# Optimization experiments

Hardware: AMD Instinct MI355X
Metric: run time of the kernel (lower is better)

Reference implementation:

```python
import jax, jax.numpy as jnp
import numpy as np

D = 512   # d_model
K = 24    # decode steps
B = 8192  # batch


def setup_inputs() -> dict:
    key = jax.random.key(0)
    ks = jax.random.split(key, 10)
    s = 1.0 / np.sqrt(D)
    return {
        "initial": jax.random.normal(ks[0], (B, 1, 1), jnp.float32),
        "encoder_hidden": jax.random.normal(ks[1], (B, D), jnp.float32) * 0.1,
        "encoder_cell": jax.random.normal(ks[2], (B, D), jnp.float32) * 0.1,
        # LSTM params: input dim is 1 (feedback of dense1 output); gate order i,f,g,o (Keras)
        "Wx": jax.random.normal(ks[3], (1, 4 * D), jnp.float32) * s,
        "Wu": jax.random.normal(ks[4], (D, 4 * D), jnp.float32) * s,
        "b": jnp.zeros((4 * D,), jnp.float32),
        "w1": jax.random.normal(ks[5], (D, 1), jnp.float32) * s,
        "b1": jnp.zeros((1,), jnp.float32),
        "w2": jax.random.normal(ks[6], (D, 1), jnp.float32) * s,
        "b2": jnp.zeros((1,), jnp.float32),
    }


def reference(initial, encoder_hidden, encoder_cell, Wx, Wu, b, w1, b1, w2, b2):
    """Autoregressive LSTM decode: step 0 consumes `initial`, then feeds dense1
    output back as the next LSTM input; state carries across all K steps."""

    def step(carry, _):
        x, h, c = carry                      # x:[B,1], h,c:[B,D]
        z = x @ Wx + h @ Wu + b              # [B,4D]
        i, f, g, o = jnp.split(z, 4, axis=-1)
        i = jax.nn.sigmoid(i)
        f = jax.nn.sigmoid(f)
        g = jnp.tanh(g)
        o = jax.nn.sigmoid(o)
        c = f * c + i * g
        h = o * jnp.tanh(c)
        y1 = jax.nn.sigmoid(h @ w1 + b1)     # dense1, feedback input
        y2 = jax.nn.elu(h @ w2 + b2)         # dense2
        return (y1, h, c), (y1, y2)

    x0 = initial[:, 0, :]                    # [B,1]
    _, (ys1, ys2) = jax.lax.scan(step, (x0, encoder_hidden, encoder_cell), None, length=K)
    out1 = jnp.transpose(ys1[..., 0], (1, 0))  # [B,K]
    out2 = jnp.transpose(ys2[..., 0], (1, 0))  # [B,K]
    return out1, out2
```

## Files before the change

### kernel.cpp

```cpp
#include <hip/hip_runtime.h>

#define D_ 512
#define ND_ 2048
#define KS_ 24
#define TB_ 32
#define B_ 8192
#define NU_ 33

typedef __attribute__((ext_vector_type(8))) short short8;
typedef __attribute__((ext_vector_type(16))) float f32x16;
typedef unsigned short u16;

#define SWZ(row, kb) (((row) * 1024) + ((kb) ^ (((row) & 15) << 4)))

__device__ __forceinline__ u16 f2bf(float f) {
  union { float f; unsigned int u; } v; v.f = f;
  unsigned int u = v.u;
  return (u16)((u + 0x7FFFu + ((u >> 16) & 1u)) >> 16);
}

__device__ __forceinline__ float sigm(float x) { return 1.0f / (1.0f + __expf(-x)); }
__device__ __forceinline__ float tanh_(float x) {
  float e = __expf(2.0f * x);
  return (e - 1.0f) / (e + 1.0f);
}

__device__ __forceinline__ void glds16(const u16* g, void* l) {
  __builtin_amdgcn_global_load_lds(
      (const __attribute__((address_space(1))) unsigned int*)g,
      (__attribute__((address_space(3))) unsigned int*)l, 16, 0, 0);
}

__global__ __launch_bounds__(256) void pack_wu_kernel(const float* __restrict__ Wu,
                                                      const float* __restrict__ Wx,
                                                      const float* __restrict__ b,
                                                      u16* __restrict__ pk) {
  int idx = blockIdx.x * 256 + threadIdx.x;
  int lane = idx & 63;
  int unit = idx >> 6;
  if (unit >= 64 * NU_) return;
  int nt = unit / NU_;
  int un = unit - nt * NU_;
  int col = nt * 32 + (lane & 31);
  u16 t[8] = {0, 0, 0, 0, 0, 0, 0, 0};
  if (un < 32) {
    int k0 = un * 16 + (lane >> 5) * 8;
#pragma unroll
    for (int j = 0; j < 8; ++j) t[j] = f2bf(Wu[(size_t)(k0 + j) * ND_ + col]);
  } else if ((lane >> 5) == 0) {
    t[0] = f2bf(Wx[col]);
    t[1] = f2bf(b[col]);
  }
  int4 w;
  w.x = t[0] | (t[1] << 16); w.y = t[2] | (t[3] << 16);
  w.z = t[4] | (t[5] << 16); w.w = t[6] | (t[7] << 16);
  *reinterpret_cast<int4*>(pk + (size_t)unit * 512 + lane * 8) = w;
}

__global__ __launch_bounds__(1024, 4) void lstm_kernel(
    const float* __restrict__ initial, const float* __restrict__ enc_h,
    const float* __restrict__ enc_c,
    const float* __restrict__ w1, const float* __restrict__ b1,
    const float* __restrict__ w2, const float* __restrict__ b2,
    const u16* __restrict__ wu, float* __restrict__ out) {
  __shared__ __align__(16) unsigned char hbuf[2][TB_ * 1024];
  __shared__ __align__(16) unsigned char wu_stage[16 * 4096];
  __shared__ float x_lds[TB_];
  __shared__ float ly1[16][TB_];
  __shared__ float ly2[16][TB_];

  const int tid = threadIdx.x;
  const int wv  = tid >> 6;
  const int wvu = __builtin_amdgcn_readfirstlane(wv);
  const int l   = tid & 63;
  const int l31 = l & 31;
  const int lhi = l >> 5;
  const int b0  = blockIdx.x * TB_;

  {
    int row = tid >> 5;
    int seg = tid & 31;
    const float* src = enc_h + (size_t)(b0 + row) * D_ + seg * 16;
#pragma unroll
    for (int jb = 0; jb < 2; ++jb) {
      u16 t[8];
#pragma unroll
      for (int j = 0; j < 8; ++j) t[j] = f2bf(src[jb * 8 + j]);
      int kb = seg * 32 + jb * 16;
      int4 w;
      w.x = t[0] | (t[1] << 16); w.y = t[2] | (t[3] << 16);
      w.z = t[4] | (t[5] << 16); w.w = t[6] | (t[7] << 16);
      *reinterpret_cast<int4*>(&hbuf[0][SWZ(row, kb)]) = w;
    }
  }
  if (tid < TB_) x_lds[tid] = initial[b0 + tid];

  const int col = wvu * 32 + l31;
  const float w1v = w1[col], w2v = w2[col];
  const float b1v = b1[0], b2v = b2[0];

  float creg[16];
#pragma unroll
  for (int r = 0; r < 16; ++r) {
    const int row = (r & 3) + 8 * (r >> 2) + 4 * lhi;
    creg[r] = enc_c[(size_t)(b0 + row) * D_ + col];
  }

  const u16* wb0 = wu + (size_t)(( 0 + wvu) * NU_) * 512;
  const u16* wb1 = wu + (size_t)((16 + wvu) * NU_) * 512;
  const u16* wb2 = wu + (size_t)((32 + wvu) * NU_) * 512;
  const u16* wb3 = wu + (size_t)((48 + wvu) * NU_) * 512;
  const size_t lofs8 = (size_t)l * 8;

  unsigned char* stg = &wu_stage[wvu * 4096];
  const int lofs = l * 16;
  const int abase = lhi * 16;

  __syncthreads();

  for (int s = 0; s < KS_; ++s) {
    const unsigned char* hr = hbuf[s & 1];
    unsigned char* hw = hbuf[(s & 1) ^ 1];

    f32x16 acc0 = {}, acc1 = {}, acc2 = {}, acc3 = {};

    glds16(wb0 + lofs8, stg);
    glds16(wb1 + lofs8, stg + 1024);

#pragma unroll 1
    for (int ks = 0; ks <= 32; ++ks) {
      const size_t o = (size_t)ks * 512 + lofs8;
      glds16(wb2 + o, stg + 2048);
      glds16(wb3 + o, stg + 3072);
      asm volatile("s_waitcnt vmcnt(2)" ::: "memory");
      short8 a;
      if (ks < 32) {
        a = *reinterpret_cast<const short8*>(&hr[SWZ(l31, ks * 32 + abase)]);
      } else {
        short8 z8 = {};
        a = z8;
        if (lhi == 0) {
          a[0] = (short)f2bf(x_lds[l31]);
          a[1] = (short)0x3F80;
        }
      }
      short8 f0 = *reinterpret_cast<const short8*>(stg + lofs);
      short8 f1 = *reinterpret_cast<const short8*>(stg + 1024 + lofs);
      acc0 = __builtin_amdgcn_mfma_f32_32x32x16_bf16(a, f0, acc0, 0, 0, 0);
      acc1 = __builtin_amdgcn_mfma_f32_32x32x16_bf16(a, f1, acc1, 0, 0, 0);
      if (ks < 32) {
        const size_t o2 = (size_t)(ks + 1) * 512 + lofs8;
        glds16(wb0 + o2, stg);
        glds16(wb1 + o2, stg + 1024);
        asm volatile("s_waitcnt vmcnt(2)" ::: "memory");
      } else {
        asm volatile("s_waitcnt vmcnt(0)" ::: "memory");
      }
      short8 f2 = *reinterpret_cast<const short8*>(stg + 2048 + lofs);
      short8 f3 = *reinterpret_cast<const short8*>(stg + 3072 + lofs);
      acc2 = __builtin_amdgcn_mfma_f32_32x32x16_bf16(a, f2, acc2, 0, 0, 0);
      acc3 = __builtin_amdgcn_mfma_f32_32x32x16_bf16(a, f3, acc3, 0, 0, 0);
    }

#pragma unroll
    for (int rb = 0; rb < 16; rb += 4) {
      float y1t[4], y2t[4];
#pragma unroll
      for (int q = 0; q < 4; ++q) {
        const int r = rb + q;
        const int row = (r & 3) + 8 * (r >> 2) + 4 * lhi;
        float ig = sigm(acc0[r]);
        float fg = sigm(acc1[r]);
        float gg = tanh_(acc2[r]);
        float og = sigm(acc3[r]);
        float cn = fg * creg[r] + ig * gg;
        creg[r] = cn;
        float hn = og * tanh_(cn);
        *reinterpret_cast<u16*>(&hw[SWZ(row, col * 2)]) = f2bf(hn);
        y1t[q] = hn * w1v;
        y2t[q] = hn * w2v;
      }
#pragma unroll
      for (int m = 1; m < 32; m <<= 1) {
#pragma unroll
        for (int q = 0; q < 4; ++q) {
          y1t[q] += __shfl_xor(y1t[q], m);
          y2t[q] += __shfl_xor(y2t[q], m);
        }
      }
      if (l31 == 0) {
#pragma unroll
        for (int q = 0; q < 4; ++q) {
          const int r = rb + q;
          const int row = (r & 3) + 8 * (r >> 2) + 4 * lhi;
          ly1[wvu][row] = y1t[q];
          ly2[wvu][row] = y2t[q];
        }
      }
    }
    __syncthreads();

    if (tid < TB_) {
      float s1 = b1v, s2 = b2v;
#pragma unroll
      for (int wq = 0; wq < 16; ++wq) { s1 += ly1[wq][tid]; s2 += ly2[wq][tid]; }
      float y1 = sigm(s1);
      float y2 = (s2 > 0.f) ? s2 : (__expf(s2) - 1.0f);
      out[(size_t)(b0 + tid) * KS_ + s] = y1;
      out[(size_t)B_ * KS_ + (size_t)(b0 + tid) * KS_ + s] = y2;
      x_lds[tid] = y1;
    }
    __syncthreads();
  }
}

extern "C" void kernel_launch(void* const* d_in, const int* in_sizes, int n_in,
                              void* d_out, int out_size, void* d_ws, size_t ws_size,
                              hipStream_t stream) {
  const float* initial = (const float*)d_in[0];
  const float* enc_h   = (const float*)d_in[1];
  const float* enc_c   = (const float*)d_in[2];
  const float* Wx      = (const float*)d_in[3];
  const float* Wu      = (const float*)d_in[4];
  const float* bias    = (const float*)d_in[5];
  const float* w1      = (const float*)d_in[6];
  const float* b1      = (const float*)d_in[7];
  const float* w2      = (const float*)d_in[8];
  const float* b2      = (const float*)d_in[9];
  u16* pk = (u16*)d_ws;

  pack_wu_kernel<<<528, 256, 0, stream>>>(Wu, Wx, bias, pk);
  lstm_kernel<<<256, 1024, 0, stream>>>(initial, enc_h, enc_c, w1, b1,
                                        w2, b2, pk, (float*)d_out);
}
```

Measured before the change: 834.8 us.

## Halve waves per block, two column tiles per wave, deeper continuous weight prefetch ring

Each block now runs 8 waves instead of 16, and each wave handles two 32-column tiles in sequence, A then B. Weight staging becomes a 5-slot ring buffer per wave, and prefetch runs continuously across the passes and decode steps, so the next tile's weights are already loading at the end of each pass. The dense-head partial sums are reduced once per step over both tiles, with half as many LDS partials. This aims to hide global weight-load latency with deeper prefetch and to cut the number of waves taking part in barriers. In exchange it doubles the serial work per wave, uses more registers for two cell-state arrays and the partial-sum arrays, and relies on carefully tracked vmcnt counts.

```diff
diff --git a/kernel.cpp b/kernel.cpp
--- a/kernel.cpp
+++ b/kernel.cpp
@@ -57,17 +57,73 @@
   *reinterpret_cast<int4*>(pk + (size_t)unit * 512 + lane * 8) = w;
 }
 
-__global__ __launch_bounds__(1024, 4) void lstm_kernel(
+#define KSTEP_PASS(CREG, COL, W1V, W2V, A0, A1, A2, A3, X0, X1, X2, X3)        \
+  {                                                                            \
+    acc0 = (f32x16){}; acc1 = (f32x16){}; acc2 = (f32x16){}; acc3 = (f32x16){};\
+    _Pragma("unroll 1")                                                        \
+    for (int ks = 0; ks < 33; ++ks) {                                          \
+      int iks = ks + 2; int swp = 0;                                           \
+      if (iks >= 33) { iks -= 33; swp = 1; }                                   \
+      const size_t io = (size_t)iks * 512 + lofs8;                             \
+                        \
+      glds16((swp ? X0 : A0) + io, stg + slot_i * 2048);                       \
+      glds16((swp ? X1 : A1) + io, stg + slot_i * 2048 + 1024);                \
+      slot_i = (slot_i == 4) ? 0 : slot_i + 1;                                 \
+      asm volatile("s_waitcnt vmcnt(8)" ::: "memory");                         \
+      short8 a;                                                                \
+      if (ks < 32) {                                                           \
+        a = *reinterpret_cast<const short8*>(&hr[SWZ(l31, ks * 32 + abase)]);  \
+      } else {                                                                 \
+        short8 z8 = {};                                                        \
+        if (lhi == 0) {                                                        \
+          z8[0] = (short)f2bf(x_lds[l31]);                                     \
+          z8[1] = (short)0x3F80;                                               \
+        }                                                                      \
+        a = z8;                                                                \
+      }                                                                        \
+      short8 f0 = *reinterpret_cast<const short8*>(stg + slot_c * 2048 + lofs);\
+      short8 f1 = *reinterpret_cast<const short8*>(stg + slot_c * 2048 + 1024 + lofs);\
+      slot_c = (slot_c == 4) ? 0 : slot_c + 1;                                 \
+      acc0 = __builtin_amdgcn_mfma_f32_32x32x16_bf16(a, f0, acc0, 0, 0, 0);    \
+      acc1 = __builtin_amdgcn_mfma_f32_32x32x16_bf16(a, f1, acc1, 0, 0, 0);    \
+                                                                     \
+      glds16((swp ? X2 : A2) + io, stg + slot_i * 2048);                       \
+      glds16((swp ? X3 : A3) + io, stg + slot_i * 2048 + 1024);                \
+      slot_i = (slot_i == 4) ? 0 : slot_i + 1;                                 \
+      asm volatile("s_waitcnt vmcnt(8)" ::: "memory");                         \
+      short8 f2 = *reinterpret_cast<const short8*>(stg + slot_c * 2048 + lofs);\
+      short8 f3 = *reinterpret_cast<const short8*>(stg + slot_c * 2048 + 1024 + lofs);\
+      slot_c = (slot_c == 4) ? 0 : slot_c + 1;                                 \
+      acc2 = __builtin_amdgcn_mfma_f32_32x32x16_bf16(a, f2, acc2, 0, 0, 0);    \
+      acc3 = __builtin_amdgcn_mfma_f32_32x32x16_bf16(a, f3, acc3, 0, 0, 0);    \
+    }                                                                          \
+    _Pragma("unroll")                                                          \
+    for (int r = 0; r < 16; ++r) {                                             \
+      const int row = (r & 3) + 8 * (r >> 2) + 4 * lhi;                        \
+      float ig = sigm(acc0[r]);                                                \
+      float fg = sigm(acc1[r]);                                                \
+      float gg = tanh_(acc2[r]);                                               \
+      float og = sigm(acc3[r]);                                                \
+      float cn = fg * CREG[r] + ig * gg;                                       \
+      CREG[r] = cn;                                                            \
+      float hn = og * tanh_(cn);                                               \
+      *reinterpret_cast<u16*>(&hw[SWZ(row, (COL) * 2)]) = f2bf(hn);            \
+      y1p[r] += hn * (W1V);                                                    \
+      y2p[r] += hn * (W2V);                                                    \
+    }                                                                          \
+  }
+
+__global__ __launch_bounds__(512, 2) void lstm_kernel(
     const float* __restrict__ initial, const float* __restrict__ enc_h,
     const float* __restrict__ enc_c,
     const float* __restrict__ w1, const float* __restrict__ b1,
     const float* __restrict__ w2, const float* __restrict__ b2,
     const u16* __restrict__ wu, float* __restrict__ out) {
   __shared__ __align__(16) unsigned char hbuf[2][TB_ * 1024];
-  __shared__ __align__(16) unsigned char wu_stage[16 * 4096];
+  __shared__ __align__(16) unsigned char wu_stage[8 * 5 * 2048];
   __shared__ float x_lds[TB_];
-  __shared__ float ly1[16][TB_];
-  __shared__ float ly2[16][TB_];
+  __shared__ float ly1[8][TB_];
+  __shared__ float ly2[8][TB_];
 
   const int tid = threadIdx.x;
   const int wv  = tid >> 6;
@@ -78,15 +134,15 @@
   const int b0  = blockIdx.x * TB_;
 
   {
-    int row = tid >> 5;
-    int seg = tid & 31;
-    const float* src = enc_h + (size_t)(b0 + row) * D_ + seg * 16;
-#pragma unroll
-    for (int jb = 0; jb < 2; ++jb) {
+    int row = tid >> 4;
+    int seg = tid & 15;
+    const float* src = enc_h + (size_t)(b0 + row) * D_ + seg * 32;
+#pragma unroll
+    for (int jb = 0; jb < 4; ++jb) {
       u16 t[8];
 #pragma unroll
       for (int j = 0; j < 8; ++j) t[j] = f2bf(src[jb * 8 + j]);
-      int kb = seg * 32 + jb * 16;
+      int kb = seg * 64 + jb * 16;
       int4 w;
       w.x = t[0] | (t[1] << 16); w.y = t[2] | (t[3] << 16);
       w.z = t[4] | (t[5] << 16); w.w = t[6] | (t[7] << 16);
@@ -95,107 +151,72 @@
   }
   if (tid < TB_) x_lds[tid] = initial[b0 + tid];
 
-  const int col = wvu * 32 + l31;
-  const float w1v = w1[col], w2v = w2[col];
+  const int colA = wvu * 32 + l31;
+  const int colB = (8 + wvu) * 32 + l31;
+  const float w1vA = w1[colA], w1vB = w1[colB];
+  const float w2vA = w2[colA], w2vB = w2[colB];
   const float b1v = b1[0], b2v = b2[0];
 
-  float creg[16];
+  float cregA[16], cregB[16];
 #pragma unroll
   for (int r = 0; r < 16; ++r) {
     const int row = (r & 3) + 8 * (r >> 2) + 4 * lhi;
-    creg[r] = enc_c[(size_t)(b0 + row) * D_ + col];
-  }
-
-  const u16* wb0 = wu + (size_t)(( 0 + wvu) * NU_) * 512;
-  const u16* wb1 = wu + (size_t)((16 + wvu) * NU_) * 512;
-  const u16* wb2 = wu + (size_t)((32 + wvu) * NU_) * 512;
-  const u16* wb3 = wu + (size_t)((48 + wvu) * NU_) * 512;
+    cregA[r] = enc_c[(size_t)(b0 + row) * D_ + colA];
+    cregB[r] = enc_c[(size_t)(b0 + row) * D_ + colB];
+  }
+
+  const u16* wA0 = wu + (size_t)(( 0 + wvu) * NU_) * 512;
+  const u16* wA1 = wu + (size_t)((16 + wvu) * NU_) * 512;
+  const u16* wA2 = wu + (size_t)((32 + wvu) * NU_) * 512;
+  const u16* wA3 = wu + (size_t)((48 + wvu) * NU_) * 512;
+  const u16* wB0 = wu + (size_t)(( 8 + wvu) * NU_) * 512;
+  const u16* wB1 = wu + (size_t)((24 + wvu) * NU_) * 512;
+  const u16* wB2 = wu + (size_t)((40 + wvu) * NU_) * 512;
+  const u16* wB3 = wu + (size_t)((56 + wvu) * NU_) * 512;
   const size_t lofs8 = (size_t)l * 8;
-
-  unsigned char* stg = &wu_stage[wvu * 4096];
   const int lofs = l * 16;
   const int abase = lhi * 16;
+  unsigned char* stg = &wu_stage[wvu * 10240];
 
   __syncthreads();
+  asm volatile("s_waitcnt vmcnt(0)" ::: "memory");
+
+  glds16(wA0 + lofs8, stg);
+  glds16(wA1 + lofs8, stg + 1024);
+  glds16(wA2 + lofs8, stg + 2048);
+  glds16(wA3 + lofs8, stg + 3072);
+  glds16(wA0 + 512 + lofs8, stg + 4096);
+  glds16(wA1 + 512 + lofs8, stg + 5120);
+  glds16(wA2 + 512 + lofs8, stg + 6144);
+  glds16(wA3 + 512 + lofs8, stg + 7168);
+  int slot_i = 4, slot_c = 0;
 
   for (int s = 0; s < KS_; ++s) {
     const unsigned char* hr = hbuf[s & 1];
     unsigned char* hw = hbuf[(s & 1) ^ 1];
 
-    f32x16 acc0 = {}, acc1 = {}, acc2 = {}, acc3 = {};
-
-    glds16(wb0 + lofs8, stg);
-    glds16(wb1 + lofs8, stg + 1024);
-
-#pragma unroll 1
-    for (int ks = 0; ks <= 32; ++ks) {
-      const size_t o = (size_t)ks * 512 + lofs8;
-      glds16(wb2 + o, stg + 2048);
-      glds16(wb3 + o, stg + 3072);
-      asm volatile("s_waitcnt vmcnt(2)" ::: "memory");
-      short8 a;
-      if (ks < 32) {
-        a = *reinterpret_cast<const short8*>(&hr[SWZ(l31, ks * 32 + abase)]);
-      } else {
-        short8 z8 = {};
-        a = z8;
-        if (lhi == 0) {
-          a[0] = (short)f2bf(x_lds[l31]);
-          a[1] = (short)0x3F80;
-        }
+    float y1p[16], y2p[16];
+#pragma unroll
+    for (int r = 0; r < 16; ++r) { y1p[r] = 0.f; y2p[r] = 0.f; }
+
+    f32x16 acc0, acc1, acc2, acc3;
+    KSTEP_PASS(cregA, colA, w1vA, w2vA, wA0, wA1, wA2, wA3, wB0, wB1, wB2, wB3)
+    KSTEP_PASS(cregB, colB, w1vB, w2vB, wB0, wB1, wB2, wB3, wA0, wA1, wA2, wA3)
+
+#pragma unroll
+    for (int m = 1; m < 32; m <<= 1) {
+#pragma unroll
+      for (int r = 0; r < 16; ++r) {
+        y1p[r] += __shfl_xor(y1p[r], m);
+        y2p[r] += __shfl_xor(y2p[r], m);
       }
-      short8 f0 = *reinterpret_cast<const short8*>(stg + lofs);
-      short8 f1 = *reinterpret_cast<const short8*>(stg + 1024 + lofs);
-      acc0 = __builtin_amdgcn_mfma_f32_32x32x16_bf16(a, f0, acc0, 0, 0, 0);
-      acc1 = __builtin_amdgcn_mfma_f32_32x32x16_bf16(a, f1, acc1, 0, 0, 0);
-      if (ks < 32) {
-        const size_t o2 = (size_t)(ks + 1) * 512 + lofs8;
-        glds16(wb0 + o2, stg);
-        glds16(wb1 + o2, stg + 1024);
-        asm volatile("s_waitcnt vmcnt(2)" ::: "memory");
-      } else {
-        asm volatile("s_waitcnt vmcnt(0)" ::: "memory");
-      }
-      short8 f2 = *reinterpret_cast<const short8*>(stg + 2048 + lofs);
-      short8 f3 = *reinterpret_cast<const short8*>(stg + 3072 + lofs);
-      acc2 = __builtin_amdgcn_mfma_f32_32x32x16_bf16(a, f2, acc2, 0, 0, 0);
-      acc3 = __builtin_amdgcn_mfma_f32_32x32x16_bf16(a, f3, acc3, 0, 0, 0);
-    }
-
-#pragma unroll
-    for (int rb = 0; rb < 16; rb += 4) {
-      float y1t[4], y2t[4];
-#pragma unroll
-      for (int q = 0; q < 4; ++q) {
-        const int r = rb + q;
+    }
+    if (l31 == 0) {
+#pragma unroll
+      for (int r = 0; r < 16; ++r) {
         const int row = (r & 3) + 8 * (r >> 2) + 4 * lhi;
-        float ig = sigm(acc0[r]);
-        float fg = sigm(acc1[r]);
-        float gg = tanh_(acc2[r]);
-        float og = sigm(acc3[r]);
-        float cn = fg * creg[r] + ig * gg;
-        creg[r] = cn;
-        float hn = og * tanh_(cn);
-        *reinterpret_cast<u16*>(&hw[SWZ(row, col * 2)]) = f2bf(hn);
-        y1t[q] = hn * w1v;
-        y2t[q] = hn * w2v;
-      }
-#pragma unroll
-      for (int m = 1; m < 32; m <<= 1) {
-#pragma unroll
-        for (int q = 0; q < 4; ++q) {
-          y1t[q] += __shfl_xor(y1t[q], m);
-          y2t[q] += __shfl_xor(y2t[q], m);
-        }
-      }
-      if (l31 == 0) {
-#pragma unroll
-        for (int q = 0; q < 4; ++q) {
-          const int r = rb + q;
-          const int row = (r & 3) + 8 * (r >> 2) + 4 * lhi;
-          ly1[wvu][row] = y1t[q];
-          ly2[wvu][row] = y2t[q];
-        }
+        ly1[wvu][row] = y1p[r];
+        ly2[wvu][row] = y2p[r];
       }
     }
     __syncthreads();
@@ -203,7 +224,7 @@
     if (tid < TB_) {
       float s1 = b1v, s2 = b2v;
 #pragma unroll
-      for (int wq = 0; wq < 16; ++wq) { s1 += ly1[wq][tid]; s2 += ly2[wq][tid]; }
+      for (int wq = 0; wq < 8; ++wq) { s1 += ly1[wq][tid]; s2 += ly2[wq][tid]; }
       float y1 = sigm(s1);
       float y2 = (s2 > 0.f) ? s2 : (__expf(s2) - 1.0f);
       out[(size_t)(b0 + tid) * KS_ + s] = y1;
@@ -230,6 +251,6 @@
   u16* pk = (u16*)d_ws;
 
   pack_wu_kernel<<<528, 256, 0, stream>>>(Wu, Wx, bias, pk);
-  lstm_kernel<<<256, 1024, 0, stream>>>(initial, enc_h, enc_c, w1, b1,
-                                        w2, b2, pk, (float*)d_out);
-}
+  lstm_kernel<<<256, 512, 0, stream>>>(initial, enc_h, enc_c, w1, b1,
+                                       w2, b2, pk, (float*)d_out);
+}
```

Result: slower. 874.3 us (+4.7%).

## Load Wu fragments directly into registers and move cell state to LDS

Applied to the files above, without the earlier changes.

Replaces the global_load_lds staging of packed Wu tiles with direct register loads, double-buffered across two k-slices and prefetched for the next step after the GEMM. The cell state moves from 16 registers into a shared-memory array to free registers for the extra fragment buffers. The epilogue now processes two rows per shuffle-reduction group instead of four. This removes LDS staging traffic and per-iteration waitcnt stalls, at the cost of more VGPR pressure and extra LDS reads and writes for the cell state.

```diff
diff --git a/kernel.cpp b/kernel.cpp
--- a/kernel.cpp
+++ b/kernel.cpp
@@ -23,12 +23,6 @@
 __device__ __forceinline__ float tanh_(float x) {
   float e = __expf(2.0f * x);
   return (e - 1.0f) / (e + 1.0f);
-}
-
-__device__ __forceinline__ void glds16(const u16* g, void* l) {
-  __builtin_amdgcn_global_load_lds(
-      (const __attribute__((address_space(1))) unsigned int*)g,
-      (__attribute__((address_space(3))) unsigned int*)l, 16, 0, 0);
 }
 
 __global__ __launch_bounds__(256) void pack_wu_kernel(const float* __restrict__ Wu,
@@ -57,6 +51,14 @@
   *reinterpret_cast<int4*>(pk + (size_t)unit * 512 + lane * 8) = w;
 }
 
+#define LD8(P, u) (*reinterpret_cast<const short8*>((P) + (size_t)(u) * 512 + lofs8))
+#define AH(ks) (*reinterpret_cast<const short8*>(&hr[SWZ(l31, (ks) * 32 + abase)]))
+#define MFMA_(A, B, C) __builtin_amdgcn_mfma_f32_32x32x16_bf16(A, B, C, 0, 0, 0)
+
+#define KPRO(P0, P1, P2, P3)                                                   \
+    fA0 = LD8(P0, 0); fA1 = LD8(P1, 0); fA2 = LD8(P2, 0); fA3 = LD8(P3, 0);    \
+    fB0 = LD8(P0, 1); fB1 = LD8(P1, 1); fB2 = LD8(P2, 1); fB3 = LD8(P3, 1);
+
 __global__ __launch_bounds__(1024, 4) void lstm_kernel(
     const float* __restrict__ initial, const float* __restrict__ enc_h,
     const float* __restrict__ enc_c,
@@ -64,7 +66,7 @@
     const float* __restrict__ w2, const float* __restrict__ b2,
     const u16* __restrict__ wu, float* __restrict__ out) {
   __shared__ __align__(16) unsigned char hbuf[2][TB_ * 1024];
-  __shared__ __align__(16) unsigned char wu_stage[16 * 4096];
+  __shared__ float c_lds[TB_][D_];
   __shared__ float x_lds[TB_];
   __shared__ float ly1[16][TB_];
   __shared__ float ly2[16][TB_];
@@ -92,89 +94,79 @@
       w.z = t[4] | (t[5] << 16); w.w = t[6] | (t[7] << 16);
       *reinterpret_cast<int4*>(&hbuf[0][SWZ(row, kb)]) = w;
     }
+    const float* csrc = enc_c + (size_t)(b0 + row) * D_ + seg * 16;
+    float* cdst = &c_lds[row][seg * 16];
+#pragma unroll
+    for (int j = 0; j < 16; j += 4)
+      *reinterpret_cast<float4*>(cdst + j) = *reinterpret_cast<const float4*>(csrc + j);
   }
   if (tid < TB_) x_lds[tid] = initial[b0 + tid];
 
   const int col = wvu * 32 + l31;
   const float w1v = w1[col], w2v = w2[col];
-  const float b1v = b1[0], b2v = b2[0];
-
-  float creg[16];
-#pragma unroll
-  for (int r = 0; r < 16; ++r) {
-    const int row = (r & 3) + 8 * (r >> 2) + 4 * lhi;
-    creg[r] = enc_c[(size_t)(b0 + row) * D_ + col];
-  }
-
-  const u16* wb0 = wu + (size_t)(( 0 + wvu) * NU_) * 512;
-  const u16* wb1 = wu + (size_t)((16 + wvu) * NU_) * 512;
-  const u16* wb2 = wu + (size_t)((32 + wvu) * NU_) * 512;
-  const u16* wb3 = wu + (size_t)((48 + wvu) * NU_) * 512;
+
+  const u16* s0 = wu + (size_t)(( 0 + wvu) * NU_) * 512;
+  const u16* s1 = wu + (size_t)((16 + wvu) * NU_) * 512;
+  const u16* s2 = wu + (size_t)((32 + wvu) * NU_) * 512;
+  const u16* s3 = wu + (size_t)((48 + wvu) * NU_) * 512;
   const size_t lofs8 = (size_t)l * 8;
-
-  unsigned char* stg = &wu_stage[wvu * 4096];
-  const int lofs = l * 16;
   const int abase = lhi * 16;
 
   __syncthreads();
+
+  short8 fA0, fA1, fA2, fA3, fB0, fB1, fB2, fB3;
+  f32x16 acc0, acc1, acc2, acc3;
+
+  KPRO(s0, s1, s2, s3)
 
   for (int s = 0; s < KS_; ++s) {
     const unsigned char* hr = hbuf[s & 1];
     unsigned char* hw = hbuf[(s & 1) ^ 1];
 
-    f32x16 acc0 = {}, acc1 = {}, acc2 = {}, acc3 = {};
-
-    glds16(wb0 + lofs8, stg);
-    glds16(wb1 + lofs8, stg + 1024);
+    acc0 = (f32x16){}; acc1 = (f32x16){}; acc2 = (f32x16){}; acc3 = (f32x16){};
 
 #pragma unroll 1
-    for (int ks = 0; ks <= 32; ++ks) {
-      const size_t o = (size_t)ks * 512 + lofs8;
-      glds16(wb2 + o, stg + 2048);
-      glds16(wb3 + o, stg + 3072);
-      asm volatile("s_waitcnt vmcnt(2)" ::: "memory");
-      short8 a;
-      if (ks < 32) {
-        a = *reinterpret_cast<const short8*>(&hr[SWZ(l31, ks * 32 + abase)]);
-      } else {
-        short8 z8 = {};
-        a = z8;
-        if (lhi == 0) {
-          a[0] = (short)f2bf(x_lds[l31]);
-          a[1] = (short)0x3F80;
-        }
-      }
-      short8 f0 = *reinterpret_cast<const short8*>(stg + lofs);
-      short8 f1 = *reinterpret_cast<const short8*>(stg + 1024 + lofs);
-      acc0 = __builtin_amdgcn_mfma_f32_32x32x16_bf16(a, f0, acc0, 0, 0, 0);
-      acc1 = __builtin_amdgcn_mfma_f32_32x32x16_bf16(a, f1, acc1, 0, 0, 0);
-      if (ks < 32) {
-        const size_t o2 = (size_t)(ks + 1) * 512 + lofs8;
-        glds16(wb0 + o2, stg);
-        glds16(wb1 + o2, stg + 1024);
-        asm volatile("s_waitcnt vmcnt(2)" ::: "memory");
-      } else {
-        asm volatile("s_waitcnt vmcnt(0)" ::: "memory");
-      }
-      short8 f2 = *reinterpret_cast<const short8*>(stg + 2048 + lofs);
-      short8 f3 = *reinterpret_cast<const short8*>(stg + 3072 + lofs);
-      acc2 = __builtin_amdgcn_mfma_f32_32x32x16_bf16(a, f2, acc2, 0, 0, 0);
-      acc3 = __builtin_amdgcn_mfma_f32_32x32x16_bf16(a, f3, acc3, 0, 0, 0);
-    }
-
-#pragma unroll
-    for (int rb = 0; rb < 16; rb += 4) {
-      float y1t[4], y2t[4];
-#pragma unroll
-      for (int q = 0; q < 4; ++q) {
+    for (int ks = 0; ks < 30; ks += 2) {
+      short8 a0 = AH(ks);
+      acc0 = MFMA_(a0, fA0, acc0); acc1 = MFMA_(a0, fA1, acc1);
+      acc2 = MFMA_(a0, fA2, acc2); acc3 = MFMA_(a0, fA3, acc3);
+      fA0 = LD8(s0, ks + 2); fA1 = LD8(s1, ks + 2);
+      fA2 = LD8(s2, ks + 2); fA3 = LD8(s3, ks + 2);
+      short8 a1 = AH(ks + 1);
+      acc0 = MFMA_(a1, fB0, acc0); acc1 = MFMA_(a1, fB1, acc1);
+      acc2 = MFMA_(a1, fB2, acc2); acc3 = MFMA_(a1, fB3, acc3);
+      fB0 = LD8(s0, ks + 3); fB1 = LD8(s1, ks + 3);
+      fB2 = LD8(s2, ks + 3); fB3 = LD8(s3, ks + 3);
+    }
+    {
+      short8 a0 = AH(30);
+      acc0 = MFMA_(a0, fA0, acc0); acc1 = MFMA_(a0, fA1, acc1);
+      acc2 = MFMA_(a0, fA2, acc2); acc3 = MFMA_(a0, fA3, acc3);
+      fA0 = LD8(s0, 32); fA1 = LD8(s1, 32);
+      fA2 = LD8(s2, 32); fA3 = LD8(s3, 32);
+      short8 a1 = AH(31);
+      acc0 = MFMA_(a1, fB0, acc0); acc1 = MFMA_(a1, fB1, acc1);
+      acc2 = MFMA_(a1, fB2, acc2); acc3 = MFMA_(a1, fB3, acc3);
+      short8 ax = {};
+      if (lhi == 0) { ax[0] = (short)f2bf(x_lds[l31]); ax[1] = (short)0x3F80; }
+      acc0 = MFMA_(ax, fA0, acc0); acc1 = MFMA_(ax, fA1, acc1);
+      acc2 = MFMA_(ax, fA2, acc2); acc3 = MFMA_(ax, fA3, acc3);
+    }
+    KPRO(s0, s1, s2, s3)
+
+#pragma unroll
+    for (int rb = 0; rb < 16; rb += 2) {
+      float y1t[2], y2t[2];
+#pragma unroll
+      for (int q = 0; q < 2; ++q) {
         const int r = rb + q;
         const int row = (r & 3) + 8 * (r >> 2) + 4 * lhi;
         float ig = sigm(acc0[r]);
         float fg = sigm(acc1[r]);
         float gg = tanh_(acc2[r]);
         float og = sigm(acc3[r]);
-        float cn = fg * creg[r] + ig * gg;
-        creg[r] = cn;
+        float cn = fg * c_lds[row][col] + ig * gg;
+        c_lds[row][col] = cn;
         float hn = og * tanh_(cn);
         *reinterpret_cast<u16*>(&hw[SWZ(row, col * 2)]) = f2bf(hn);
         y1t[q] = hn * w1v;
@@ -183,14 +175,14 @@
 #pragma unroll
       for (int m = 1; m < 32; m <<= 1) {
 #pragma unroll
-        for (int q = 0; q < 4; ++q) {
+        for (int q = 0; q < 2; ++q) {
           y1t[q] += __shfl_xor(y1t[q], m);
           y2t[q] += __shfl_xor(y2t[q], m);
         }
       }
       if (l31 == 0) {
 #pragma unroll
-        for (int q = 0; q < 4; ++q) {
+        for (int q = 0; q < 2; ++q) {
           const int r = rb + q;
           const int row = (r & 3) + 8 * (r >> 2) + 4 * lhi;
           ly1[wvu][row] = y1t[q];
@@ -201,11 +193,11 @@
     __syncthreads();
 
     if (tid < TB_) {
-      float s1 = b1v, s2 = b2v;
-#pragma unroll
-      for (int wq = 0; wq < 16; ++wq) { s1 += ly1[wq][tid]; s2 += ly2[wq][tid]; }
-      float y1 = sigm(s1);
-      float y2 = (s2 > 0.f) ? s2 : (__expf(s2) - 1.0f);
+      float s1v = b1[0], s2v = b2[0];
+#pragma unroll
+      for (int wq = 0; wq < 16; ++wq) { s1v += ly1[wq][tid]; s2v += ly2[wq][tid]; }
+      float y1 = sigm(s1v);
+      float y2 = (s2v > 0.f) ? s2v : (__expf(s2v) - 1.0f);
       out[(size_t)(b0 + tid) * KS_ + s] = y1;
       out[(size_t)B_ * KS_ + (size_t)(b0 + tid) * KS_ + s] = y2;
       x_lds[tid] = y1;
```

New measurement: 909.8 us. 9.0% more time.
